# Kernel tuning notes

Measured on AMD Instinct MI355X. Metric: run time of the kernel, lower is better.

The kernel has to match this reference:

```python
import jax, jax.numpy as jnp
import numpy as np
from functools import partial

EDGES = [(1,2),(1,3),(1,4),(1,5),(1,6),(2,3),(2,7),(2,8),(3,4),(3,9),(4,5),(4,10),(5,6),(5,11),(6,12),(6,13),(7,8),(7,14),(8,9),(8,14),(9,10),(9,15),(10,11),(10,16),(11,12),(11,17),(12,13),(12,18),(13,18),(14,15),(14,19),(15,16),(15,19),(16,17),(16,20),(17,18),(17,21),(18,21),(19,20),(19,22),(20,21),(20,22),(21,22),(24,25),(24,29),(25,26),(25,29),(26,17),(26,30),(27,28),(27,31),(28,31),(29,30),(29,32),(30,31),(30,32),(31,32),(34,35),(34,39),(35,36),(35,39),(36,37),(36,30),(37,18),(37,41),(38,41),(39,40),(39,42),(30,41),(30,42),(31,42),(44,45),(44,49),(45,46),(45,49),(46,47),(46,50),(47,48),(47,51),(48,51),(49,50),(49,52),(50,51),(50,52),(51,52),(54,55),(54,59),(55,56),(55,59),(56,57),(56,60),(57,58),(57,61),(58,61),(59,60),(59,62),(50,61),(60,62),(61,62)]

B, C, T = 32, 64, 4000
F1, D, F2, NCLS = 8, 2, 16, 4
KLEN, GK = 64, 8


def _bn_pack(k, c):
    kg, kb = jax.random.split(k)
    g = jax.random.uniform(kg, (c,), minval=0.5, maxval=1.5)
    b = 0.1 * jax.random.normal(kb, (c,))
    return jnp.stack([g, b, jnp.zeros(c), jnp.ones(c)])  # gamma, beta, mean, var


def setup_inputs() -> dict:
    key = jax.random.key(0)
    ks = jax.random.split(key, 16)
    A = np.zeros((C, C), np.float32)
    for i, j in EDGES:
        A[i - 1, j - 1] = 1.0
        A[j - 1, i - 1] = 1.0
    np.fill_diagonal(A, 1.0)
    feat = F2 * ((T // 4 + 1) // 8)  # 16 * 125 = 2000
    s = 0.1
    return {
        "x": jax.random.normal(ks[0], (B, C, T), jnp.float32),
        "adjacency": jnp.asarray(A),
        "conv1_w": s * jax.random.normal(ks[1], (F1, 1, 1, KLEN), jnp.float32),
        "bnF1": jnp.stack([_bn_pack(jax.random.fold_in(ks[2], i), F1) for i in range(4)]),
        "imp": jax.random.normal(ks[3], (3, F1, C, C), jnp.float32),
        "gconv_w": s * jax.random.normal(ks[4], (3, F1, F1, 1, GK), jnp.float32),
        "dw_w": s * jax.random.normal(ks[5], (F1 * D, 1, C, 1), jnp.float32),
        "bn_sp": _bn_pack(ks[6], F1 * D),
        "sep_dw_w": s * jax.random.normal(ks[7], (F1 * D, 1, 1, 16), jnp.float32),
        "sep_pw_w": s * jax.random.normal(ks[8], (F2, F1 * D, 1, 1), jnp.float32),
        "bn_sep": _bn_pack(ks[9], F2),
        "fc_w": s * jax.random.normal(ks[10], (NCLS, feat), jnp.float32),
        "fc_b": jnp.zeros((NCLS,), jnp.float32),
    }


def _conv(x, w, pad, groups=1):
    return jax.lax.conv_general_dilated(
        x, w, (1, 1), pad, dimension_numbers=("NCHW", "OIHW", "NCHW"),
        feature_group_count=groups)


def _bn(x, p, eps=1e-3):
    g, b, m, v = p
    scale = g * jax.lax.rsqrt(v + eps)
    return x * scale[None, :, None, None] + (b - m * scale)[None, :, None, None]


def reference(x, adjacency, conv1_w, bnF1, imp, gconv_w, dw_w, bn_sp,
              sep_dw_w, sep_pw_w, bn_sep, fc_w, fc_b):
    Bv = x.shape[0]
    h = x[:, None, :, :]                                    # (B,1,C,T)
    h = _conv(h, conv1_w, [(0, 0), (31, 32)])                # 'same' for k=64
    h = _bn(h, bnF1[0])
    for l in range(3):                                       # GraphTemporalConvolution x3
        A = adjacency[None] * imp[l]                         # (F1,C,C) masked importance
        h = jnp.einsum("fcd,bfdt->bfct", A, h)
        h = _conv(h, gconv_w[l], [(0, 0), (3, 4)])           # 'same' for k=8
        h = jax.nn.elu(_bn(h, bnF1[l + 1]))
    # spatial depthwise conv with max-norm constraint (renorm, no grad through scale)
    norms = jnp.sqrt(jnp.sum(dw_w ** 2, axis=(1, 2, 3), keepdims=True))
    scale = jax.lax.stop_gradient(jnp.minimum(1.0, 1.0 / jnp.maximum(norms, 1e-7)))
    h = _conv(h, dw_w * scale, [(0, 0), (0, 0)], groups=F1)  # (B,F1*D,1,T)
    h = jax.nn.elu(_bn(h, bn_sp))
    h = h.reshape(Bv, F1 * D, 1, T // 4, 4).mean(-1)         # AvgPool (1,4)
    # separable conv
    h = _conv(h, sep_dw_w, [(0, 0), (8, 8)], groups=F1 * D)  # width T/4 + 1
    h = _conv(h, sep_pw_w, [(0, 0), (0, 0)])
    h = jax.nn.elu(_bn(h, bn_sep))
    W = h.shape[-1]
    Wp = (W // 8) * 8
    h = h[..., :Wp].reshape(Bv, F2, 1, Wp // 8, 8).mean(-1)  # AvgPool (1,8)
    feat = h.reshape(Bv, -1)
    return feat @ fc_w.T + fc_b
```

## Files before the change

### kernel.cpp

```cpp
#include <hip/hip_runtime.h>


#define B_   32
#define C_   64
#define T_   4000
#define F1_  8
#define TP_  1000
#define W2_  1001
#define MAXDEG 16
#define ROW4 130
#define ROWD 520

typedef _Float16 h16x2 __attribute__((ext_vector_type(2)));
typedef _Float16 f16x8 __attribute__((ext_vector_type(8)));
typedef float    f32x4 __attribute__((ext_vector_type(4)));
typedef __fp16   cvt16x2 __attribute__((ext_vector_type(2)));

static __device__ __forceinline__ float bf2f(unsigned short h) {
  union { unsigned int u; float f; } v; v.u = ((unsigned int)h) << 16; return v.f;
}
static __device__ __forceinline__ unsigned short f2bf(float f) {
  union { float f; unsigned int u; } v; v.f = f;
  unsigned int r = v.u + 0x7FFFu + ((v.u >> 16) & 1u);
  return (unsigned short)(r >> 16);
}
static __device__ __forceinline__ float lo_h(unsigned int u) {
  union { unsigned int u; _Float16 h[2]; } v; v.u = u; return (float)v.h[0];
}
static __device__ __forceinline__ unsigned int pack2h(float a, float b) {
  union { _Float16 h[2]; unsigned int u; } v;
  v.h[0] = (_Float16)a; v.h[1] = (_Float16)b; return v.u;
}
#if defined(__has_builtin) && __has_builtin(__builtin_amdgcn_cvt_pkrtz)
static __device__ __forceinline__ unsigned int pkh(float a, float b) {
  union { cvt16x2 h; unsigned int u; } v;
  v.h = __builtin_amdgcn_cvt_pkrtz(a, b);
  return v.u;
}
#else
static __device__ __forceinline__ unsigned int pkh(float a, float b) {
  return pack2h(a, b);
}
#endif
static __device__ __forceinline__ h16x2 as_h2(unsigned int u) {
  union { unsigned int u; h16x2 h; } v; v.u = u; return v.h;
}
static __device__ __forceinline__ unsigned int alignb(unsigned int hi,
                                                      unsigned int lo,
                                                      unsigned int s) {
  return (unsigned int)(((((unsigned long long)hi) << 32) | lo) >> s);
}
static __device__ __forceinline__ float swz8(float v) {
  union { float f; int i; } a; a.f = v;
  a.i = __builtin_amdgcn_ds_swizzle(a.i, 0x201F);
  return a.f;
}
#define PERM_LO(y, x) __builtin_amdgcn_perm((y), (x), 0x05040100u)
#define PERM_HI(y, x) __builtin_amdgcn_perm((y), (x), 0x07060302u)
#if defined(__has_builtin) && __has_builtin(__builtin_amdgcn_fdot2)
#define DOT2(a, b, c) __builtin_amdgcn_fdot2((a), (b), (c), false)
#else
static __device__ __forceinline__ float dot2_fb(h16x2 a, h16x2 b, float c) {
  return fmaf((float)a[0], (float)b[0], fmaf((float)a[1], (float)b[1], c));
}
#define DOT2(a, b, c) dot2_fb((a), (b), (c))
#endif
static __device__ __forceinline__ float eluf(float z) {
  return z > 0.0f ? z : __expf(z) - 1.0f;
}
static __device__ __forceinline__ float ldin(const void* p, int i, int isf32) {
  return isf32 ? ((const float*)p)[i] : bf2f(((const unsigned short*)p)[i]);
}

__global__ __launch_bounds__(256) void k0_setup(
    const void* __restrict__ adj, const void* __restrict__ imp,
    const void* __restrict__ dww, const void* __restrict__ w1,
    const void* __restrict__ bnF, const void* __restrict__ gw,
    const void* __restrict__ bnsp, const void* __restrict__ sdw,
    const void* __restrict__ pw, const void* __restrict__ bnsep,
    const void* __restrict__ fcw, const void* __restrict__ fcb,
    int* __restrict__ flag, int* __restrict__ deg, int* __restrict__ col,
    float* __restrict__ avals, unsigned int* __restrict__ w1h,
    uint4* __restrict__ wmf, float* __restrict__ dwn,
    float* __restrict__ sdwc, float* __restrict__ pwc,
    float* __restrict__ fcwc, float* __restrict__ fcbc,
    float* __restrict__ bnFs, float* __restrict__ bnsps,
    float* __restrict__ bnseps,
    unsigned int* __restrict__ avph,
    unsigned int* __restrict__ dwph)
{
  __shared__ float dwr[1024];
  __shared__ float dsc[16];
  int tid = threadIdx.x;
  int isf32 = (((const float*)adj)[0] == 1.0f) ? 1 : 0;
  if (tid == 0) *flag = isf32;

  for (int idx = tid; idx < 256; idx += 256) {
    int f = idx >> 5, p = idx & 31;
    w1h[idx] = pack2h(ldin(w1, f*64 + 2*p, isf32), ldin(w1, f*64 + 2*p + 1, isf32));
  }
  for (int idx = tid; idx < 384; idx += 256) {
    int lf = idx >> 6;
    int layer = lf >> 1, frag = lf & 1;
    int lane2 = idx & 63;
    int o = lane2 & 15, ii = (lane2 >> 4) + 4*frag;
    uint4 v; v.x = 0u; v.y = 0u; v.z = 0u; v.w = 0u;
    if (o < 8) {
      int bi = layer*512 + (o*8 + ii)*8;
      v.x = pack2h(ldin(gw, bi+0, isf32), ldin(gw, bi+1, isf32));
      v.y = pack2h(ldin(gw, bi+2, isf32), ldin(gw, bi+3, isf32));
      v.z = pack2h(ldin(gw, bi+4, isf32), ldin(gw, bi+5, isf32));
      v.w = pack2h(ldin(gw, bi+6, isf32), ldin(gw, bi+7, isf32));
    }
    wmf[idx] = v;
  }
  for (int i = tid; i < 256;  i += 256) sdwc[i] = ldin(sdw, i, isf32);
  for (int i = tid; i < 256;  i += 256) pwc[i]  = ldin(pw, i, isf32);
  for (int i = tid; i < 8000; i += 256) fcwc[i] = ldin(fcw, i, isf32);
  if (tid < 4) fcbc[tid] = ldin(fcb, tid, isf32);
  for (int i = tid; i < 1024; i += 256) dwr[i] = ldin(dww, i, isf32);

  if (tid < 64) {
    int c = tid, n = 0;
    for (int e = 0; e < MAXDEG; ++e) col[c*MAXDEG + e] = c;
    for (int d = 0; d < 64; ++d) {
      if (ldin(adj, c*64 + d, isf32) != 0.0f) {
        if (n < MAXDEG) col[c*MAXDEG + n] = d;
        ++n;
      }
    }
    deg[c] = n < MAXDEG ? n : MAXDEG;
  }
  __syncthreads();
  if (tid < 16) {
    float s2 = 0.0f;
    for (int c2 = 0; c2 < 64; ++c2) { float wv = dwr[tid*64 + c2]; s2 += wv*wv; }
    dsc[tid] = fminf(1.0f, 1.0f / fmaxf(sqrtf(s2), 1e-7f));
  }
  if (tid >= 64 && tid < 96) {
    int i = tid - 64, s = i >> 3, f = i & 7;
    float g = ldin(bnF, s*32 + f,      isf32);
    float b = ldin(bnF, s*32 + 8 + f,  isf32);
    float m = ldin(bnF, s*32 + 16 + f, isf32);
    float v = ldin(bnF, s*32 + 24 + f, isf32);
    float sc = g * rsqrtf(v + 1e-3f);
    bnFs[s*16 + f] = sc; bnFs[s*16 + 8 + f] = b - m*sc;
  }
  if (tid >= 96 && tid < 112) {
    int ch = tid - 96;
    float g = ldin(bnsp, ch, isf32), b = ldin(bnsp, 16 + ch, isf32);
    float m = ldin(bnsp, 32 + ch, isf32), v = ldin(bnsp, 48 + ch, isf32);
    float sc = g * rsqrtf(v + 1e-3f);
    bnsps[ch] = sc; bnsps[16 + ch] = b - m*sc;
  }
  if (tid >= 112 && tid < 128) {
    int ch = tid - 112;
    float g = ldin(bnsep, ch, isf32), b = ldin(bnsep, 16 + ch, isf32);
    float m = ldin(bnsep, 32 + ch, isf32), v = ldin(bnsep, 48 + ch, isf32);
    float sc = g * rsqrtf(v + 1e-3f);
    bnseps[ch] = sc; bnseps[16 + ch] = b - m*sc;
  }
  for (int combo = tid; combo < 3*8*64; combo += 256) {
    int l = combo >> 9, f = (combo >> 6) & 7, c = combo & 63;
    int dg = deg[c];
    for (int e = 0; e < MAXDEG; ++e) {
      float v = 0.0f;
      if (e < dg) {
        int d = col[c*MAXDEG + e];
        v = ldin(adj, c*64 + d, isf32) * ldin(imp, ((l*8 + f)*64 + c)*64 + d, isf32);
      }
      avals[((l*8 + f)*64 + c)*MAXDEG + e] = v;
    }
  }
  __syncthreads();
  for (int i = tid; i < 1024; i += 256) dwn[i] = dwr[i] * dsc[i >> 6];
  for (int idx = tid; idx < 3*8*64*8; idx += 256) {
    int base16 = (idx >> 3) * MAXDEG, p = idx & 7;
    avph[idx] = pack2h(avals[base16 + 2*p], avals[base16 + 2*p + 1]);
  }
  __syncthreads();
  for (int idx = tid; idx < 512; idx += 256) {
    int ch = idx >> 5, p = idx & 31;
    dwph[idx] = pack2h(dwn[ch*64 + 2*p], dwn[ch*64 + 2*p + 1]);
  }
}

__global__ __launch_bounds__(256, 4) void k1_conv1_bn(
    const void* __restrict__ x,
    const unsigned int* __restrict__ w1h,
    const float* __restrict__ bnFs,
    const int* __restrict__ flag,
    unsigned short* __restrict__ outp)
{
  __shared__ __align__(16) unsigned int xs[548];
  int tid = threadIdx.x;
  int bc = blockIdx.y;
  int b = bc >> 6, c = bc & 63;
  int tb = blockIdx.x * 1024;
  int isf32 = *flag;
  int row = bc * T_;
  if (isf32) {
    const float* xr = (const float*)x + row;
    for (int m = tid; m < 274; m += 256) {
      int tg = tb - 36 + 4*m;
      uint2 st;
      if (tg >= 0 && tg + 3 < T_) {
        float4 v = *(const float4*)(xr + tg);
        st.x = pkh(v.x, v.y); st.y = pkh(v.z, v.w);
      } else {
        float q0 = (tg   >= 0 && tg   < T_) ? xr[tg]   : 0.0f;
        float q1 = (tg+1 >= 0 && tg+1 < T_) ? xr[tg+1] : 0.0f;
        float q2 = (tg+2 >= 0 && tg+2 < T_) ? xr[tg+2] : 0.0f;
        float q3 = (tg+3 >= 0 && tg+3 < T_) ? xr[tg+3] : 0.0f;
        st.x = pkh(q0, q1); st.y = pkh(q2, q3);
      }
      *(uint2*)(xs + 2*m) = st;
    }
  } else {
    const unsigned short* xr = (const unsigned short*)x + row;
    for (int m = tid; m < 274; m += 256) {
      int tg = tb - 36 + 4*m;
      uint2 st;
      if (tg >= 0 && tg + 3 < T_) {
        uint2 v = *(const uint2*)(xr + tg);
        st.x = pkh(bf2f((unsigned short)(v.x & 0xFFFFu)),
                   bf2f((unsigned short)(v.x >> 16)));
        st.y = pkh(bf2f((unsigned short)(v.y & 0xFFFFu)),
                   bf2f((unsigned short)(v.y >> 16)));
      } else {
        float q0 = (tg   >= 0 && tg   < T_) ? bf2f(xr[tg])   : 0.0f;
        float q1 = (tg+1 >= 0 && tg+1 < T_) ? bf2f(xr[tg+1]) : 0.0f;
        float q2 = (tg+2 >= 0 && tg+2 < T_) ? bf2f(xr[tg+2]) : 0.0f;
        float q3 = (tg+3 >= 0 && tg+3 < T_) ? bf2f(xr[tg+3]) : 0.0f;
        st.x = pkh(q0, q1); st.y = pkh(q2, q3);
      }
      *(uint2*)(xs + 2*m) = st;
    }
  }
  __syncthreads();
  int t0 = tb + 4*tid;
  if (t0 >= T_) return;
  float acc[8][4];
  #pragma unroll
  for (int f = 0; f < 8; ++f)
    #pragma unroll
    for (int j = 0; j < 4; ++j) acc[f][j] = 0.0f;
  uint2 a0 = *(const uint2*)(xs + 2*tid + 2);
  uint2 a1 = *(const uint2*)(xs + 2*tid + 4);
  unsigned u0 = a0.x, u1 = a0.y, u2 = a1.x, u3 = a1.y;
  for (int cc = 0; cc < 16; ++cc) {
    unsigned od0 = alignb(u1, u0, 16);
    unsigned od1 = alignb(u2, u1, 16);
    unsigned od2 = alignb(u3, u2, 16);
    #pragma unroll
    for (int f = 0; f < 8; ++f) {
      h16x2 wa = as_h2(w1h[f*32 + 2*cc]);
      h16x2 wb = as_h2(w1h[f*32 + 2*cc + 1]);
      acc[f][0] = DOT2(as_h2(od0), wa, acc[f][0]);
      acc[f][0] = DOT2(as_h2(od1), wb, acc[f][0]);
      acc[f][1] = DOT2(as_h2(u1),  wa, acc[f][1]);
      acc[f][1] = DOT2(as_h2(u2),  wb, acc[f][1]);
      acc[f][2] = DOT2(as_h2(od1), wa, acc[f][2]);
      acc[f][2] = DOT2(as_h2(od2), wb, acc[f][2]);
      acc[f][3] = DOT2(as_h2(u2),  wa, acc[f][3]);
      acc[f][3] = DOT2(as_h2(u3),  wb, acc[f][3]);
    }
    u0 = u2; u1 = u3;
    if (cc < 15) {
      uint2 nx = *(const uint2*)(xs + 2*tid + 6 + 2*cc);
      u2 = nx.x; u3 = nx.y;
    }
  }
  #pragma unroll
  for (int f = 0; f < 8; ++f) {
    float sc = bnFs[f], sh = bnFs[8 + f];
    uint2 st;
    st.x = pkh(acc[f][0]*sc + sh, acc[f][1]*sc + sh);
    st.y = pkh(acc[f][2]*sc + sh, acc[f][3]*sc + sh);
    *(uint2*)(outp + ((b*8 + f)*64 + c)*T_ + t0) = st;
  }
}

__global__ __launch_bounds__(256, 6) void k23_gcn_gconv(
    const unsigned short* __restrict__ in,
    unsigned short* __restrict__ outp,
    const int* __restrict__ deg, const int* __restrict__ col,
    const float* __restrict__ avals,
    const unsigned int* __restrict__ avph,
    const uint4* __restrict__ wmf,
    const float* __restrict__ bnFs, int l)
{
  __shared__ __align__(16) uint4 ash[8 * ROW4];
  int tid = threadIdx.x;
  int wgid = blockIdx.y * 4 + blockIdx.x;
  int swz  = (wgid & 7) * 1024 + (wgid >> 3);
  int c = swz & 63;
  int xt = (swz >> 6) & 3;
  int b = swz >> 8;
  int tb = xt * 1024;
  int wb = tb - 8;
  int dg = deg[c];
  const int* cp = col + c*MAXDEG;

  {
    int i = tid >> 5;
    int mlane = tid & 31;
    int dgp = (dg + 1) >> 1;
    const unsigned int* wpp = avph + ((l*8 + i)*64 + c) * 8;
    const float* av = avals + ((l*8 + i)*64 + c) * MAXDEG;
    const unsigned short* rbp = in + (size_t)((b*8 + i) * 64) * T_;
    for (int m = mlane; m < ROW4; m += 32) {
      int t = wb + 8*m;
      float a[8] = {0,0,0,0,0,0,0,0};
      if (t >= 0 && t + 7 < T_) {
        for (int p = 0; p < dgp; ++p) {
          int d0 = cp[2*p];
          int d1 = cp[2*p + 1];
          h16x2 w2 = as_h2(wpp[p]);
          uint4 v0 = *(const uint4*)(rbp + d0*T_ + t);
          uint4 v1 = *(const uint4*)(rbp + d1*T_ + t);
          a[0] = DOT2(as_h2(PERM_LO(v1.x, v0.x)), w2, a[0]);
          a[1] = DOT2(as_h2(PERM_HI(v1.x, v0.x)), w2, a[1]);
          a[2] = DOT2(as_h2(PERM_LO(v1.y, v0.y)), w2, a[2]);
          a[3] = DOT2(as_h2(PERM_HI(v1.y, v0.y)), w2, a[3]);
          a[4] = DOT2(as_h2(PERM_LO(v1.z, v0.z)), w2, a[4]);
          a[5] = DOT2(as_h2(PERM_HI(v1.z, v0.z)), w2, a[5]);
          a[6] = DOT2(as_h2(PERM_LO(v1.w, v0.w)), w2, a[6]);
          a[7] = DOT2(as_h2(PERM_HI(v1.w, v0.w)), w2, a[7]);
        }
      } else if (t + 7 >= 0 && t < T_) {
        for (int e = 0; e < dg; ++e) {
          int d = cp[e];
          float wv = av[e];
          const unsigned short* rp = rbp + d*T_;
          #pragma unroll
          for (int q = 0; q < 8; ++q) {
            int tq = t + q;
            if (tq >= 0 && tq < T_)
              a[q] = fmaf(wv, lo_h((unsigned int)rp[tq]), a[q]);
          }
        }
      }
      uint4 o;
      o.x = pkh(a[0], a[1]); o.y = pkh(a[2], a[3]);
      o.z = pkh(a[4], a[5]); o.w = pkh(a[6], a[7]);
      ash[i*ROW4 + m] = o;
    }
  }
  __syncthreads();

  int lane = tid & 63;
  int wv4 = tid >> 6;
  int m = lane & 15, q = lane >> 4;
  int sel = (m >> 3) & 1;
  union { uint4 u; f16x8 h; } w0u, w1u;
  w0u.u = wmf[(l*2 + 0)*64 + lane];
  w1u.u = wmf[(l*2 + 1)*64 + lane];
  int o8 = m & 7;
  float sc  = bnFs[(l+1)*16 + o8];
  float shb = bnFs[(l+1)*16 + 8 + o8];
  const unsigned int* ashd = (const unsigned int*)ash;
  const unsigned int* p0 = ashd + q*ROWD + wv4*128 + m + 2;
  const unsigned int* p1 = p0 + 4*ROWD;
  unsigned short* orow = outp + (size_t)((b*8 + o8)*64 + c) * T_;
  #pragma unroll
  for (int s = 0; s < 8; ++s) {
    unsigned dwa[5], dwb[5];
    #pragma unroll
    for (int j = 0; j < 5; ++j) {
      dwa[j] = p0[16*s + j];
      dwb[j] = p1[16*s + j];
    }
    union { unsigned d[4]; f16x8 h; } Ae0, Ao0, Ae1, Ao1;
    #pragma unroll
    for (int j = 0; j < 4; ++j) {
      Ao0.d[j] = dwa[j+1];
      Ae0.d[j] = alignb(dwa[j+1], dwa[j], 16);
      Ao1.d[j] = dwb[j+1];
      Ae1.d[j] = alignb(dwb[j+1], dwb[j], 16);
    }
    f32x4 ae = {0.0f, 0.0f, 0.0f, 0.0f};
    f32x4 ao = {0.0f, 0.0f, 0.0f, 0.0f};
    ae = __builtin_amdgcn_mfma_f32_16x16x32_f16(Ae0.h, w0u.h, ae, 0, 0, 0);
    ae = __builtin_amdgcn_mfma_f32_16x16x32_f16(Ae1.h, w1u.h, ae, 0, 0, 0);
    ao = __builtin_amdgcn_mfma_f32_16x16x32_f16(Ao0.h, w0u.h, ao, 0, 0, 0);
    ao = __builtin_amdgcn_mfma_f32_16x16x32_f16(Ao1.h, w1u.h, ao, 0, 0, 0);
    float r0 = swz8(ae[2]);
    float r1 = swz8(ao[2]);
    float r2 = swz8(ae[3]);
    float r3 = swz8(ao[3]);
    float y0 = sel ? r0 : ae[0];
    float y1 = sel ? r1 : ao[0];
    float y2 = sel ? r2 : ae[1];
    float y3 = sel ? r3 : ao[1];
    int t0g = tb + wv4*256 + s*32 + 8*q + 4*sel;
    if (t0g < T_) {
      uint2 st;
      st.x = pkh(eluf(y0*sc + shb), eluf(y1*sc + shb));
      st.y = pkh(eluf(y2*sc + shb), eluf(y3*sc + shb));
      *(uint2*)(orow + t0g) = st;
    }
  }
}

__global__ __launch_bounds__(256) void k4_dw(
    const unsigned short* __restrict__ in,
    const unsigned int* __restrict__ dwph,
    const float* __restrict__ bnsps,
    float* __restrict__ p1)
{
  int tid = threadIdx.x;
  int bg = blockIdx.y;
  int b = bg >> 3, g = bg & 7;
  int tile = blockIdx.x * 256 + tid;
  if (tile >= 500) return;
  int t0 = tile * 8;
  int base = bg * (64 * T_);
  const unsigned int* w0pp = dwph + (2*g)*32;
  const unsigned int* w1pp = dwph + (2*g + 1)*32;
  float a0[8] = {0,0,0,0,0,0,0,0}, a1[8] = {0,0,0,0,0,0,0,0};
  for (int p = 0; p < 32; ++p) {
    h16x2 w02 = as_h2(w0pp[p]);
    h16x2 w12 = as_h2(w1pp[p]);
    uint4 v0 = *(const uint4*)(in + base + (2*p)*T_ + t0);
    uint4 v1 = *(const uint4*)(in + base + (2*p + 1)*T_ + t0);
    unsigned pr;
    pr = PERM_LO(v1.x, v0.x);
    a0[0] = DOT2(as_h2(pr), w02, a0[0]); a1[0] = DOT2(as_h2(pr), w12, a1[0]);
    pr = PERM_HI(v1.x, v0.x);
    a0[1] = DOT2(as_h2(pr), w02, a0[1]); a1[1] = DOT2(as_h2(pr), w12, a1[1]);
    pr = PERM_LO(v1.y, v0.y);
    a0[2] = DOT2(as_h2(pr), w02, a0[2]); a1[2] = DOT2(as_h2(pr), w12, a1[2]);
    pr = PERM_HI(v1.y, v0.y);
    a0[3] = DOT2(as_h2(pr), w02, a0[3]); a1[3] = DOT2(as_h2(pr), w12, a1[3]);
    pr = PERM_LO(v1.z, v0.z);
    a0[4] = DOT2(as_h2(pr), w02, a0[4]); a1[4] = DOT2(as_h2(pr), w12, a1[4]);
    pr = PERM_HI(v1.z, v0.z);
    a0[5] = DOT2(as_h2(pr), w02, a0[5]); a1[5] = DOT2(as_h2(pr), w12, a1[5]);
    pr = PERM_LO(v1.w, v0.w);
    a0[6] = DOT2(as_h2(pr), w02, a0[6]); a1[6] = DOT2(as_h2(pr), w12, a1[6]);
    pr = PERM_HI(v1.w, v0.w);
    a0[7] = DOT2(as_h2(pr), w02, a0[7]); a1[7] = DOT2(as_h2(pr), w12, a1[7]);
  }
  float sc0 = bnsps[2*g],     sh0 = bnsps[16 + 2*g];
  float sc1 = bnsps[2*g + 1], sh1 = bnsps[16 + 2*g + 1];
  int oi = t0 >> 2;
  float2 r0, r1;
  r0.x = 0.25f * (eluf(a0[0]*sc0+sh0) + eluf(a0[1]*sc0+sh0)
                + eluf(a0[2]*sc0+sh0) + eluf(a0[3]*sc0+sh0));
  r0.y = 0.25f * (eluf(a0[4]*sc0+sh0) + eluf(a0[5]*sc0+sh0)
                + eluf(a0[6]*sc0+sh0) + eluf(a0[7]*sc0+sh0));
  r1.x = 0.25f * (eluf(a1[0]*sc1+sh1) + eluf(a1[1]*sc1+sh1)
                + eluf(a1[2]*sc1+sh1) + eluf(a1[3]*sc1+sh1));
  r1.y = 0.25f * (eluf(a1[4]*sc1+sh1) + eluf(a1[5]*sc1+sh1)
                + eluf(a1[6]*sc1+sh1) + eluf(a1[7]*sc1+sh1));
  *(float2*)(p1 + (b*16 + 2*g)*TP_ + oi)     = r0;
  *(float2*)(p1 + (b*16 + 2*g + 1)*TP_ + oi) = r1;
}

__global__ __launch_bounds__(256) void k5_sep(
    const float* __restrict__ p1,
    const float* __restrict__ sdwc,
    const float* __restrict__ pwc,
    const float* __restrict__ bnseps,
    float* __restrict__ p2)
{
  __shared__ float ps[16*272];
  int tid = threadIdx.x;
  int wq = blockIdx.x, b = blockIdx.y;
  int wb = wq * 256;
  for (int ch = 0; ch < 16; ++ch) {
    for (int s = tid; s < 272; s += 256) {
      int t = wb - 8 + s;
      ps[ch*272 + s] = (t >= 0 && t < TP_) ? p1[(b*16 + ch)*TP_ + t] : 0.0f;
    }
  }
  __syncthreads();
  int w0 = wb + tid;
  if (w0 >= W2_) return;
  float dws[16];
  for (int ch = 0; ch < 16; ++ch) {
    float a = 0.0f;
    #pragma unroll
    for (int k = 0; k < 16; ++k)
      a = fmaf(sdwc[ch*16 + k], ps[ch*272 + tid + k], a);
    dws[ch] = a;
  }
  for (int f = 0; f < 16; ++f) {
    float a = 0.0f;
    #pragma unroll
    for (int ch = 0; ch < 16; ++ch) a = fmaf(pwc[f*16 + ch], dws[ch], a);
    float sc = bnseps[f], sh = bnseps[16 + f];
    p2[(b*16 + f)*W2_ + w0] = eluf(a*sc + sh);
  }
}

__global__ __launch_bounds__(256) void k6_fc(
    const float* __restrict__ p2,
    const float* __restrict__ fcwc,
    const float* __restrict__ fcbc,
    const int* __restrict__ flag,
    void* __restrict__ outp)
{
  __shared__ float red[4*256];
  int tid = threadIdx.x;
  int b = blockIdx.x;
  float part[4] = {0.0f, 0.0f, 0.0f, 0.0f};
  for (int idx = tid; idx < 2000; idx += 256) {
    int f = idx / 125, q = idx - f*125;
    const float* src = p2 + (b*16 + f)*W2_ + q*8;
    float s = src[0]+src[1]+src[2]+src[3]+src[4]+src[5]+src[6]+src[7];
    float mval = 0.125f * s;
    #pragma unroll
    for (int n = 0; n < 4; ++n) part[n] = fmaf(fcwc[n*2000 + idx], mval, part[n]);
  }
  #pragma unroll
  for (int n = 0; n < 4; ++n) red[n*256 + tid] = part[n];
  __syncthreads();
  for (int s = 128; s > 0; s >>= 1) {
    if (tid < s) {
      #pragma unroll
      for (int n = 0; n < 4; ++n) red[n*256 + tid] += red[n*256 + tid + s];
    }
    __syncthreads();
  }
  if (tid < 4) {
    float val = red[tid*256] + fcbc[tid];
    if (*flag) ((float*)outp)[b*4 + tid] = val;
    else       ((unsigned short*)outp)[b*4 + tid] = f2bf(val);
  }
}

extern "C" void kernel_launch(void* const* d_in, const int* in_sizes, int n_in,
                              void* d_out, int out_size, void* d_ws, size_t ws_size,
                              hipStream_t stream) {
  const void* x     = d_in[0];
  const void* adj   = d_in[1];
  const void* w1    = d_in[2];
  const void* bnF   = d_in[3];
  const void* imp   = d_in[4];
  const void* gw    = d_in[5];
  const void* dww   = d_in[6];
  const void* bnsp  = d_in[7];
  const void* sdw   = d_in[8];
  const void* pw    = d_in[9];
  const void* bnsep = d_in[10];
  const void* fcw   = d_in[11];
  const void* fcb   = d_in[12];

  char* w = (char*)d_ws;
  const size_t OFF = 262144000;
  unsigned short* bufA = (unsigned short*)(w);
  unsigned short* bufB = (unsigned short*)(w + 131072000);
  int*   flag   = (int*)  (w + OFF + 0);
  int*   deg    = (int*)  (w + OFF + 256);
  int*   col    = (int*)  (w + OFF + 512);
  float* avals  = (float*)(w + OFF + 4608);
  float* dwn    = (float*)(w + OFF + 108032);
  float* sdwc   = (float*)(w + OFF + 112128);
  float* pwc    = (float*)(w + OFF + 113152);
  float* fcwc   = (float*)(w + OFF + 114176);
  float* fcbc   = (float*)(w + OFF + 146176);
  float* bnFs   = (float*)(w + OFF + 146432);
  float* bnsps  = (float*)(w + OFF + 146688);
  float* bnseps = (float*)(w + OFF + 146944);
  float* p1     = (float*)(w + OFF + 147200);
  float* p2     = (float*)(w + OFF + 2195200);
  uint4* wmf    = (uint4*)(w + OFF + 4245248);
  unsigned int* avph = (unsigned int*)(w + OFF + 4251392);
  unsigned int* dwph = (unsigned int*)(w + OFF + 4300544);
  unsigned int* w1h  = (unsigned int*)(w + OFF + 4302592);

  k0_setup<<<1, 256, 0, stream>>>(adj, imp, dww, w1, bnF, gw, bnsp, sdw, pw,
                                  bnsep, fcw, fcb, flag, deg, col, avals,
                                  w1h, wmf, dwn, sdwc, pwc, fcwc, fcbc,
                                  bnFs, bnsps, bnseps, avph, dwph);
  k1_conv1_bn<<<dim3(4, B_*C_), 256, 0, stream>>>(x, w1h, bnFs, flag, bufA);
  for (int l = 0; l < 3; ++l) {
    const unsigned short* src = (l & 1) ? bufB : bufA;
    unsigned short*       dst = (l & 1) ? bufA : bufB;
    k23_gcn_gconv<<<dim3(4, B_*C_), 256, 0, stream>>>(src, dst, deg, col,
                                                      avals, avph, wmf, bnFs, l);
  }
  k4_dw<<<dim3(2, B_*F1_), 256, 0, stream>>>(bufB, dwph, bnsps, p1);
  k5_sep<<<dim3(4, B_), 256, 0, stream>>>(p1, sdwc, pwc, bnseps, p2);
  k6_fc<<<32, 256, 0, stream>>>(p2, fcwc, fcbc, flag, d_out);
}
```

Before: 514.1 us.

## Run conv1 on MFMA and split adjacency-value setup into parallel kernel

The temporal conv1 (k=64, 8 filters) is recast as 16x16x32 f16 MFMA operations. Even and odd time offsets are built from LDS with byte-align shifts, and swizzles remap the accumulator lanes to output positions. This replaces the per-thread packed dot2 loop. The weights are prepacked into an MFMA fragment layout in setup. The serial single-block computation of masked adjacency values and their f16 packing moves into a separate 6-block kernel, which shortens the setup critical path. The cost is an extra launch and more complex lane mapping, and the MFMA tiles have half the output rows padded to zero.

Result: faster. 454.2 us (-11.7%).

```diff
diff --git a/kernel.cpp b/kernel.cpp
--- a/kernel.cpp
+++ b/kernel.cpp
@@ -80,13 +80,12 @@
     const void* __restrict__ pw, const void* __restrict__ bnsep,
     const void* __restrict__ fcw, const void* __restrict__ fcb,
     int* __restrict__ flag, int* __restrict__ deg, int* __restrict__ col,
-    float* __restrict__ avals, unsigned int* __restrict__ w1h,
+    uint4* __restrict__ w1mf,
     uint4* __restrict__ wmf, float* __restrict__ dwn,
     float* __restrict__ sdwc, float* __restrict__ pwc,
     float* __restrict__ fcwc, float* __restrict__ fcbc,
     float* __restrict__ bnFs, float* __restrict__ bnsps,
     float* __restrict__ bnseps,
-    unsigned int* __restrict__ avph,
     unsigned int* __restrict__ dwph)
 {
   __shared__ float dwr[1024];
@@ -95,9 +94,18 @@
   int isf32 = (((const float*)adj)[0] == 1.0f) ? 1 : 0;
   if (tid == 0) *flag = isf32;
 
-  for (int idx = tid; idx < 256; idx += 256) {
-    int f = idx >> 5, p = idx & 31;
-    w1h[idx] = pack2h(ldin(w1, f*64 + 2*p, isf32), ldin(w1, f*64 + 2*p + 1, isf32));
+  for (int idx = tid; idx < 128; idx += 256) {
+    int kk = idx >> 6, l = idx & 63;
+    int o = l & 15, q = l >> 4;
+    uint4 v; v.x = 0u; v.y = 0u; v.z = 0u; v.w = 0u;
+    if (o < 8) {
+      int bi = o*64 + 32*kk + 8*q;
+      v.x = pack2h(ldin(w1, bi+0, isf32), ldin(w1, bi+1, isf32));
+      v.y = pack2h(ldin(w1, bi+2, isf32), ldin(w1, bi+3, isf32));
+      v.z = pack2h(ldin(w1, bi+4, isf32), ldin(w1, bi+5, isf32));
+      v.w = pack2h(ldin(w1, bi+6, isf32), ldin(w1, bi+7, isf32));
+    }
+    w1mf[idx] = v;
   }
   for (int idx = tid; idx < 384; idx += 256) {
     int lf = idx >> 6;
@@ -160,34 +168,44 @@
     float sc = g * rsqrtf(v + 1e-3f);
     bnseps[ch] = sc; bnseps[16 + ch] = b - m*sc;
   }
-  for (int combo = tid; combo < 3*8*64; combo += 256) {
-    int l = combo >> 9, f = (combo >> 6) & 7, c = combo & 63;
-    int dg = deg[c];
-    for (int e = 0; e < MAXDEG; ++e) {
-      float v = 0.0f;
-      if (e < dg) {
-        int d = col[c*MAXDEG + e];
-        v = ldin(adj, c*64 + d, isf32) * ldin(imp, ((l*8 + f)*64 + c)*64 + d, isf32);
-      }
-      avals[((l*8 + f)*64 + c)*MAXDEG + e] = v;
-    }
-  }
   __syncthreads();
   for (int i = tid; i < 1024; i += 256) dwn[i] = dwr[i] * dsc[i >> 6];
-  for (int idx = tid; idx < 3*8*64*8; idx += 256) {
-    int base16 = (idx >> 3) * MAXDEG, p = idx & 7;
-    avph[idx] = pack2h(avals[base16 + 2*p], avals[base16 + 2*p + 1]);
-  }
   __syncthreads();
   for (int idx = tid; idx < 512; idx += 256) {
     int ch = idx >> 5, p = idx & 31;
-    dwph[idx] = pack2h(dwn[ch*64 + 2*p], dwn[ch*64 + 2*p + 1]);
-  }
+    dwph[idx] = pack2h(dwr[ch*64 + 2*p]   * dsc[ch],
+                       dwr[ch*64 + 2*p+1] * dsc[ch]);
+  }
+}
+
+__global__ __launch_bounds__(256) void k0b_avals(
+    const void* __restrict__ adj, const void* __restrict__ imp,
+    const int* __restrict__ flag,
+    const int* __restrict__ deg, const int* __restrict__ col,
+    float* __restrict__ avals, unsigned int* __restrict__ avph)
+{
+  int combo = blockIdx.x * 256 + threadIdx.x;
+  int isf32 = *flag;
+  int c = combo & 63;
+  int lf = combo >> 6;
+  int dg = deg[c];
+  float av[MAXDEG];
+  for (int e = 0; e < MAXDEG; ++e) {
+    float v = 0.0f;
+    if (e < dg) {
+      int d = col[c*MAXDEG + e];
+      v = ldin(adj, c*64 + d, isf32) * ldin(imp, (lf*64 + c)*64 + d, isf32);
+    }
+    av[e] = v;
+    avals[combo*MAXDEG + e] = v;
+  }
+  for (int p = 0; p < 8; ++p)
+    avph[combo*8 + p] = pack2h(av[2*p], av[2*p + 1]);
 }
 
 __global__ __launch_bounds__(256, 4) void k1_conv1_bn(
     const void* __restrict__ x,
-    const unsigned int* __restrict__ w1h,
+    const uint4* __restrict__ w1mf,
     const float* __restrict__ bnFs,
     const int* __restrict__ flag,
     unsigned short* __restrict__ outp)
@@ -238,46 +256,56 @@
     }
   }
   __syncthreads();
-  int t0 = tb + 4*tid;
-  if (t0 >= T_) return;
-  float acc[8][4];
+
+  int lane = tid & 63;
+  int wv4 = tid >> 6;
+  int m = lane & 15, q = lane >> 4;
+  int sel = (m >> 3) & 1;
+  union { uint4 u; f16x8 h; } w0u, w1u;
+  w0u.u = w1mf[lane];
+  w1u.u = w1mf[64 + lane];
+  int o8 = m & 7;
+  float sc  = bnFs[o8];
+  float shb = bnFs[8 + o8];
+  const unsigned int* p0 = xs + 2 + m + 4*q + 128*wv4;
+  unsigned short* orow = outp + (size_t)((b*8 + o8)*64 + c) * T_;
   #pragma unroll
-  for (int f = 0; f < 8; ++f)
+  for (int s = 0; s < 8; ++s) {
+    unsigned dwa[5], dwb[5];
     #pragma unroll
-    for (int j = 0; j < 4; ++j) acc[f][j] = 0.0f;
-  uint2 a0 = *(const uint2*)(xs + 2*tid + 2);
-  uint2 a1 = *(const uint2*)(xs + 2*tid + 4);
-  unsigned u0 = a0.x, u1 = a0.y, u2 = a1.x, u3 = a1.y;
-  for (int cc = 0; cc < 16; ++cc) {
-    unsigned od0 = alignb(u1, u0, 16);
-    unsigned od1 = alignb(u2, u1, 16);
-    unsigned od2 = alignb(u3, u2, 16);
+    for (int j = 0; j < 5; ++j) {
+      dwa[j] = p0[16*s + j];
+      dwb[j] = p0[16*s + 16 + j];
+    }
+    union { unsigned d[4]; f16x8 h; } Ae0, Ao0, Ae1, Ao1;
     #pragma unroll
-    for (int f = 0; f < 8; ++f) {
-      h16x2 wa = as_h2(w1h[f*32 + 2*cc]);
-      h16x2 wb = as_h2(w1h[f*32 + 2*cc + 1]);
-      acc[f][0] = DOT2(as_h2(od0), wa, acc[f][0]);
-      acc[f][0] = DOT2(as_h2(od1), wb, acc[f][0]);
-      acc[f][1] = DOT2(as_h2(u1),  wa, acc[f][1]);
-      acc[f][1] = DOT2(as_h2(u2),  wb, acc[f][1]);
-      acc[f][2] = DOT2(as_h2(od1), wa, acc[f][2]);
-      acc[f][2] = DOT2(as_h2(od2), wb, acc[f][2]);
-      acc[f][3] = DOT2(as_h2(u2),  wa, acc[f][3]);
-      acc[f][3] = DOT2(as_h2(u3),  wb, acc[f][3]);
-    }
-    u0 = u2; u1 = u3;
-    if (cc < 15) {
-      uint2 nx = *(const uint2*)(xs + 2*tid + 6 + 2*cc);
-      u2 = nx.x; u3 = nx.y;
-    }
-  }
-  #pragma unroll
-  for (int f = 0; f < 8; ++f) {
-    float sc = bnFs[f], sh = bnFs[8 + f];
-    uint2 st;
-    st.x = pkh(acc[f][0]*sc + sh, acc[f][1]*sc + sh);
-    st.y = pkh(acc[f][2]*sc + sh, acc[f][3]*sc + sh);
-    *(uint2*)(outp + ((b*8 + f)*64 + c)*T_ + t0) = st;
+    for (int j = 0; j < 4; ++j) {
+      Ao0.d[j] = dwa[j+1];
+      Ae0.d[j] = alignb(dwa[j+1], dwa[j], 16);
+      Ao1.d[j] = dwb[j+1];
+      Ae1.d[j] = alignb(dwb[j+1], dwb[j], 16);
+    }
+    f32x4 ae = {0.0f, 0.0f, 0.0f, 0.0f};
+    f32x4 ao = {0.0f, 0.0f, 0.0f, 0.0f};
+    ae = __builtin_amdgcn_mfma_f32_16x16x32_f16(Ae0.h, w0u.h, ae, 0, 0, 0);
+    ae = __builtin_amdgcn_mfma_f32_16x16x32_f16(Ae1.h, w1u.h, ae, 0, 0, 0);
+    ao = __builtin_amdgcn_mfma_f32_16x16x32_f16(Ao0.h, w0u.h, ao, 0, 0, 0);
+    ao = __builtin_amdgcn_mfma_f32_16x16x32_f16(Ao1.h, w1u.h, ao, 0, 0, 0);
+    float r0 = swz8(ae[2]);
+    float r1 = swz8(ao[2]);
+    float r2 = swz8(ae[3]);
+    float r3 = swz8(ao[3]);
+    float y0 = sel ? r0 : ae[0];
+    float y1 = sel ? r1 : ao[0];
+    float y2 = sel ? r2 : ae[1];
+    float y3 = sel ? r3 : ao[1];
+    int t0g = tb + wv4*256 + s*32 + 8*q + 4*sel;
+    if (t0g < T_) {
+      uint2 st;
+      st.x = pkh(y0*sc + shb, y1*sc + shb);
+      st.y = pkh(y2*sc + shb, y3*sc + shb);
+      *(uint2*)(orow + t0g) = st;
+    }
   }
 }
 
@@ -569,13 +597,14 @@
   uint4* wmf    = (uint4*)(w + OFF + 4245248);
   unsigned int* avph = (unsigned int*)(w + OFF + 4251392);
   unsigned int* dwph = (unsigned int*)(w + OFF + 4300544);
-  unsigned int* w1h  = (unsigned int*)(w + OFF + 4302592);
+  uint4* w1mf   = (uint4*)(w + OFF + 4302592);
 
   k0_setup<<<1, 256, 0, stream>>>(adj, imp, dww, w1, bnF, gw, bnsp, sdw, pw,
-                                  bnsep, fcw, fcb, flag, deg, col, avals,
-                                  w1h, wmf, dwn, sdwc, pwc, fcwc, fcbc,
-                                  bnFs, bnsps, bnseps, avph, dwph);
-  k1_conv1_bn<<<dim3(4, B_*C_), 256, 0, stream>>>(x, w1h, bnFs, flag, bufA);
+                                  bnsep, fcw, fcb, flag, deg, col,
+                                  w1mf, wmf, dwn, sdwc, pwc, fcwc, fcbc,
+                                  bnFs, bnsps, bnseps, dwph);
+  k0b_avals<<<6, 256, 0, stream>>>(adj, imp, flag, deg, col, avals, avph);
+  k1_conv1_bn<<<dim3(4, B_*C_), 256, 0, stream>>>(x, w1mf, bnFs, flag, bufA);
   for (int l = 0; l < 3; ++l) {
     const unsigned short* src = (l & 1) ? bufB : bufA;
     unsigned short*       dst = (l & 1) ? bufA : bufB;
```
